# Performance work log

Hardware: AMD Instinct MI355X
Metric: run time of the kernel (lower is better)

The kernel has to match this reference:

```python
import jax, jax.numpy as jnp
import numpy as np

EPS = 1e-8
PAD = 1  # kernel // 2 for kernel=3


def setup_inputs() -> dict:
    key = jax.random.key(0)
    k1, k2, k3, k4, k5 = jax.random.split(key, 5)
    b, c, h, w = 16, 256, 64, 64
    out_ch, kernel, style_dim = 256, 3, 512
    x = jax.random.normal(k1, (b, c, h, w), dtype=jnp.float32)
    style = jax.random.normal(k2, (b, style_dim), dtype=jnp.float32)
    # learned params
    weight = jax.random.normal(k3, (1, out_ch, c, kernel, kernel), dtype=jnp.float32)
    lim = 1.0 / np.sqrt(style_dim)
    mod_w = jax.random.uniform(k4, (c, style_dim), minval=-lim, maxval=lim, dtype=jnp.float32)
    mod_b = jax.random.uniform(k5, (c,), minval=-lim, maxval=lim, dtype=jnp.float32)
    return {"x": x, "style": style, "weight": weight, "mod_w": mod_w, "mod_b": mod_b}


def reference(x, style, weight, mod_w, mod_b):
    # s[b,i]: per-sample, per-input-channel modulation from the style Linear
    s = style @ mod_w.T + mod_b                     # [b, in_ch]
    w = weight[0]                                    # [out_ch, in_ch, k, k]
    # demod factor: sum_{i,kh,kw} (w[o,i,kh,kw]*s[b,i])^2 = sum_i s^2 * sum_kk w^2
    w_sq = jnp.sum(w * w, axis=(2, 3))               # [out_ch, in_ch]
    d = jax.lax.rsqrt(jnp.einsum('oi,bi->bo', w_sq, s * s) + EPS)  # [b, out_ch]
    # modulate input channels instead of materializing per-sample weights
    xs = x * s[:, :, None, None]                     # [b, in_ch, h, w]
    y = jax.lax.conv_general_dilated(
        xs, w, window_strides=(1, 1), padding=[(PAD, PAD), (PAD, PAD)],
        dimension_numbers=('NCHW', 'OIHW', 'NCHW'))
    return y * d[:, :, None, None]                   # [b, out_ch, h, w]
```

## Files before the change

### kernel.cpp

```cpp
#include <hip/hip_runtime.h>
#include <hip/hip_bf16.h>
#include <cstdint>
#include <cstddef>

typedef __bf16 bf16_t;
typedef __bf16 bf16x4 __attribute__((ext_vector_type(4)));
typedef __bf16 bf16x8 __attribute__((ext_vector_type(8)));
typedef float  f32x4  __attribute__((ext_vector_type(4)));

#define NB   16
#define NC   256
#define NO   256
#define SD   512
#define NPIX 4096
#define CPAD 36

#define WS_S   0
#define WS_WSQ 32768
#define WS_WT  294912

__global__ __launch_bounds__(256) void prep1(
    const float* __restrict__ style, const float* __restrict__ weight,
    const float* __restrict__ mod_w, const float* __restrict__ mod_b,
    float* __restrict__ s_buf, float* __restrict__ wsq, bf16_t* __restrict__ wT)
{
    const int blk = blockIdx.x;
    const int tid = threadIdx.x;
    if (blk < 16) {
        const int b = blk, i = tid;
        const float* st = style + b * SD;
        const float* mw = mod_w + i * SD;
        float acc = 0.f;
        for (int k = 0; k < SD; k += 4) {
            float4 a = *(const float4*)(st + k);
            float4 c = *(const float4*)(mw + k);
            acc += a.x * c.x + a.y * c.y + a.z * c.z + a.w * c.w;
        }
        s_buf[b * NC + i] = acc + mod_b[i];
    } else {
        const int o = blk - 16, i = tid;
        const float* wp = weight + (o * NC + i) * 9;
        float q = 0.f;
        #pragma unroll
        for (int t = 0; t < 9; ++t) {
            float v = wp[t];
            q += v * v;
            wT[t * (NO * NC) + o * NC + i] = (bf16_t)v;
        }
        wsq[o * NC + i] = q;
    }
}

__device__ __forceinline__ void stage_a3(const bf16_t* __restrict__ wT_base,
                                         int tap0, int o0, int ic0,
                                         bf16_t* dst, int tid)
{
    #pragma unroll
    for (int t = 0; t < 3; ++t) {
        const bf16_t* wt = wT_base + (size_t)(tap0 + t) * (NO * NC);
        #pragma unroll
        for (int it = 0; it < 2; ++it) {
            int s = it * 256 + tid;
            const bf16_t* g = wt + (o0 + (s & 127)) * NC + ic0 + (s >> 7) * 8;
            __builtin_amdgcn_global_load_lds(
                (const __attribute__((address_space(1))) void*)g,
                (__attribute__((address_space(3))) void*)(dst + t * 4096 + s * 8),
                16, 0, 0);
        }
    }
}

__global__ __launch_bounds__(256, 2) void conv_mfma(
    const float* __restrict__ x,
    const bf16_t* __restrict__ wT,
    const float* __restrict__ s_buf,
    const float* __restrict__ wsq,
    float* __restrict__ out)
{
    __shared__ bf16_t lds_a[6][4096];
    __shared__ bf16_t lds_b[4 * 64 * CPAD];

    const int tid   = threadIdx.x;
    const int lane  = tid & 63;
    const int wv    = tid >> 6;
    const int wo    = wv >> 1;
    const int wp    = wv & 1;
    const int pt    = blockIdx.x;
    const int o0    = blockIdx.y * 128;
    const int batch = blockIdx.z;
    const int row0  = pt * 2;

    const int l15 = lane & 15;
    const int kg  = lane >> 4;
    const int k0  = kg * 8;

    const int colB = tid & 63;
    const int cgrp = tid >> 6;

    f32x4 acc[4][4];
    #pragma unroll
    for (int i = 0; i < 4; ++i)
        #pragma unroll
        for (int j = 0; j < 4; ++j) {
            f32x4 z = {0.f, 0.f, 0.f, 0.f};
            acc[i][j] = z;
        }

    bf16x8 bzero;
    #pragma unroll
    for (int j = 0; j < 8; ++j) bzero[j] = (bf16_t)0.f;

    bf16_t* lds_a0 = &lds_a[0][0];
    #define SUPER(idx) (lds_a0 + (size_t)((idx) & 1) * (3 * 4096))

    float vx[4][8];
    float sv[8];
    auto XLOAD = [&](int ic0) {
        const float* sp = s_buf + batch * NC + ic0 + cgrp * 8;
        float4 sa = *(const float4*)sp;
        float4 sb = *(const float4*)(sp + 4);
        sv[0]=sa.x; sv[1]=sa.y; sv[2]=sa.z; sv[3]=sa.w;
        sv[4]=sb.x; sv[5]=sb.y; sv[6]=sb.z; sv[7]=sb.w;
        const float* xbase = x + (size_t)(batch * NC + ic0 + cgrp * 8) * NPIX + colB;
        #pragma unroll
        for (int r = 0; r < 4; ++r) {
            const int gy = row0 - 1 + r;
            const bool valid = ((unsigned)gy < 64u);
            const float* rp = xbase + gy * 64;
            #pragma unroll
            for (int j = 0; j < 8; ++j)
                vx[r][j] = valid ? rp[j * NPIX] : 0.f;
        }
    };
    auto BWRITE = [&]() {
        #pragma unroll
        for (int r = 0; r < 4; ++r) {
            const int lbase = (r * 64 + colB) * CPAD + cgrp * 8;
            #pragma unroll
            for (int half = 0; half < 2; ++half) {
                union { bf16_t h[4]; uint2 u; } pk;
                #pragma unroll
                for (int j = 0; j < 4; ++j)
                    pk.h[j] = (bf16_t)(vx[r][half * 4 + j] * sv[half * 4 + j]);
                *(uint2*)&lds_b[lbase + half * 4] = pk.u;
            }
        }
    };

    stage_a3(wT, 0, o0, 0, SUPER(0), tid);
    XLOAD(0);
    BWRITE();
    __syncthreads();

    #pragma unroll 1
    for (int ch = 0; ch < 8; ++ch) {
        const int ic0 = ch * 32;

        #pragma unroll
        for (int i = 0; i < 3; ++i) {
            bf16_t* cur = SUPER(ch + i);
            bf16_t* nxt = SUPER(ch + i + 1);

            if (i < 2) {
                stage_a3(wT, 3 * (i + 1), o0, ic0, nxt, tid);
                asm volatile("s_waitcnt vmcnt(6)" ::: "memory");
            } else if (ch < 7) {
                stage_a3(wT, 0, o0, ic0 + 32, nxt, tid);
                asm volatile("s_waitcnt vmcnt(6)" ::: "memory");
            } else {
                asm volatile("s_waitcnt vmcnt(0)" ::: "memory");
            }
            __builtin_amdgcn_sched_barrier(0);

            if (i == 2 && ch < 7)
                XLOAD(ic0 + 32);

            const int r = wp + i;
            __builtin_amdgcn_s_setprio(1);
            #pragma unroll
            for (int t = 0; t < 3; ++t) {
                const bf16_t* abuf = cur + t * 4096;
                bf16x8 af[4];
                #pragma unroll
                for (int of = 0; of < 4; ++of)
                    af[of] = *(const bf16x8*)&abuf[kg * 1024 + (wo * 64 + of * 16 + l15) * 8];

                bf16x8 bfr[4];
                #pragma unroll
                for (int nf = 0; nf < 4; ++nf) {
                    const int c = nf * 16 + l15 + t - 1;
                    if ((unsigned)c < 64u) {
                        const bf16_t* p = &lds_b[(r * 64 + c) * CPAD + k0];
                        bf16x4 lo = *(const bf16x4*)p;
                        bf16x4 hi = *(const bf16x4*)(p + 4);
                        bfr[nf] = __builtin_shufflevector(lo, hi, 0, 1, 2, 3, 4, 5, 6, 7);
                    } else {
                        bfr[nf] = bzero;
                    }
                }

                #pragma unroll
                for (int of = 0; of < 4; ++of)
                    #pragma unroll
                    for (int nf = 0; nf < 4; ++nf)
                        acc[of][nf] = __builtin_amdgcn_mfma_f32_16x16x32_bf16(
                            af[of], bfr[nf], acc[of][nf], 0, 0, 0);
            }
            __builtin_amdgcn_s_setprio(0);

            if (i < 2)
                __builtin_amdgcn_s_barrier();
        }

        if (ch < 7) {
            __builtin_amdgcn_s_barrier();
            BWRITE();
            asm volatile("s_waitcnt lgkmcnt(0)" ::: "memory");
            __builtin_amdgcn_sched_barrier(0);
            __builtin_amdgcn_s_barrier();
        }
    }
    #undef SUPER

    __syncthreads();
    float* d_sh = (float*)&lds_b[0];
    {
        const int ol   = tid >> 1;
        const int half = tid & 1;
        const float* wq = wsq + (size_t)(o0 + ol) * NC + half * 128;
        const float* sb = s_buf + batch * NC + half * 128;
        float sum = 0.f;
        #pragma unroll 4
        for (int i = 0; i < 128; i += 4) {
            float4 w4 = *(const float4*)(wq + i);
            float4 s4 = *(const float4*)(sb + i);
            sum += w4.x * s4.x * s4.x + w4.y * s4.y * s4.y
                 + w4.z * s4.z * s4.z + w4.w * s4.w * s4.w;
        }
        sum += __shfl_xor(sum, 1);
        if (half == 0) d_sh[ol] = rsqrtf(sum + 1e-8f);
    }
    __syncthreads();

    const int p_base = pt * 128 + wp * 64;
    #pragma unroll
    for (int of = 0; of < 4; ++of) {
        #pragma unroll
        for (int rg = 0; rg < 4; ++rg) {
            const int o_l = wo * 64 + of * 16 + (lane >> 4) * 4 + rg;
            const float dv = d_sh[o_l];
            const size_t obase = (size_t)(batch * NO + o0 + o_l) * NPIX;
            #pragma unroll
            for (int nf = 0; nf < 4; ++nf) {
                const int p_g = p_base + nf * 16 + l15;
                out[obase + p_g] = acc[of][nf][rg] * dv;
            }
        }
    }
}

extern "C" void kernel_launch(void* const* d_in, const int* in_sizes, int n_in,
                              void* d_out, int out_size, void* d_ws, size_t ws_size,
                              hipStream_t stream)
{
    const float* x      = (const float*)d_in[0];
    const float* style  = (const float*)d_in[1];
    const float* weight = (const float*)d_in[2];
    const float* mod_w  = (const float*)d_in[3];
    const float* mod_b  = (const float*)d_in[4];
    float* out = (float*)d_out;

    char* ws = (char*)d_ws;
    float*  s_buf = (float*)(ws + WS_S);
    float*  wsq   = (float*)(ws + WS_WSQ);
    bf16_t* wT    = (bf16_t*)(ws + WS_WT);

    hipLaunchKernelGGL(prep1, dim3(272), dim3(256), 0, stream,
                       style, weight, mod_w, mod_b, s_buf, wsq, wT);
    hipLaunchKernelGGL(conv_mfma, dim3(32, 2, 16), dim3(256), 0, stream,
                       x, wT, s_buf, wsq, out);
}
```

Measured before the change: 243.1 us.

## Double block to 512 threads, splitting pixel columns across eight waves

The conv block grows from 4 to 8 wavefronts. Each wave now covers 64 output channels by 32 pixels instead of 64, which halves the accumulators and per-thread staging loads. Weight staging, x loading, the demod reduction and the epilogue are all redistributed over 512 threads, with matching vmcnt waits. This aims to raise latency hiding and lower register pressure, at the cost of more A-fragment LDS reads per MFMA and a higher launch_bounds occupancy request that may not fit LDS.

```diff
diff --git a/kernel.cpp b/kernel.cpp
--- a/kernel.cpp
+++ b/kernel.cpp
@@ -58,19 +58,16 @@
     #pragma unroll
     for (int t = 0; t < 3; ++t) {
         const bf16_t* wt = wT_base + (size_t)(tap0 + t) * (NO * NC);
-        #pragma unroll
-        for (int it = 0; it < 2; ++it) {
-            int s = it * 256 + tid;
-            const bf16_t* g = wt + (o0 + (s & 127)) * NC + ic0 + (s >> 7) * 8;
-            __builtin_amdgcn_global_load_lds(
-                (const __attribute__((address_space(1))) void*)g,
-                (__attribute__((address_space(3))) void*)(dst + t * 4096 + s * 8),
-                16, 0, 0);
-        }
-    }
-}
-
-__global__ __launch_bounds__(256, 2) void conv_mfma(
+        const int s = tid;
+        const bf16_t* g = wt + (o0 + (s & 127)) * NC + ic0 + (s >> 7) * 8;
+        __builtin_amdgcn_global_load_lds(
+            (const __attribute__((address_space(1))) void*)g,
+            (__attribute__((address_space(3))) void*)(dst + t * 4096 + s * 8),
+            16, 0, 0);
+    }
+}
+
+__global__ __launch_bounds__(512, 4) void conv_mfma(
     const float* __restrict__ x,
     const bf16_t* __restrict__ wT,
     const float* __restrict__ s_buf,
@@ -82,9 +79,10 @@
 
     const int tid   = threadIdx.x;
     const int lane  = tid & 63;
-    const int wv    = tid >> 6;
-    const int wo    = wv >> 1;
-    const int wp    = wv & 1;
+    const int wq    = tid >> 6;
+    const int wo    = wq >> 2;
+    const int prow  = (wq >> 1) & 1;
+    const int pc32  = (wq & 1) * 32;
     const int pt    = blockIdx.x;
     const int o0    = blockIdx.y * 128;
     const int batch = blockIdx.z;
@@ -97,11 +95,11 @@
     const int colB = tid & 63;
     const int cgrp = tid >> 6;
 
-    f32x4 acc[4][4];
+    f32x4 acc[4][2];
     #pragma unroll
     for (int i = 0; i < 4; ++i)
         #pragma unroll
-        for (int j = 0; j < 4; ++j) {
+        for (int j = 0; j < 2; ++j) {
             f32x4 z = {0.f, 0.f, 0.f, 0.f};
             acc[i][j] = z;
         }
@@ -113,37 +111,31 @@
     bf16_t* lds_a0 = &lds_a[0][0];
     #define SUPER(idx) (lds_a0 + (size_t)((idx) & 1) * (3 * 4096))
 
-    float vx[4][8];
-    float sv[8];
+    float vx[4][4];
+    float sv[4];
     auto XLOAD = [&](int ic0) {
-        const float* sp = s_buf + batch * NC + ic0 + cgrp * 8;
+        const float* sp = s_buf + batch * NC + ic0 + cgrp * 4;
         float4 sa = *(const float4*)sp;
-        float4 sb = *(const float4*)(sp + 4);
-        sv[0]=sa.x; sv[1]=sa.y; sv[2]=sa.z; sv[3]=sa.w;
-        sv[4]=sb.x; sv[5]=sb.y; sv[6]=sb.z; sv[7]=sb.w;
-        const float* xbase = x + (size_t)(batch * NC + ic0 + cgrp * 8) * NPIX + colB;
+        sv[0] = sa.x; sv[1] = sa.y; sv[2] = sa.z; sv[3] = sa.w;
+        const float* xbase = x + (size_t)(batch * NC + ic0 + cgrp * 4) * NPIX + colB;
         #pragma unroll
         for (int r = 0; r < 4; ++r) {
             const int gy = row0 - 1 + r;
             const bool valid = ((unsigned)gy < 64u);
             const float* rp = xbase + gy * 64;
             #pragma unroll
-            for (int j = 0; j < 8; ++j)
+            for (int j = 0; j < 4; ++j)
                 vx[r][j] = valid ? rp[j * NPIX] : 0.f;
         }
     };
     auto BWRITE = [&]() {
         #pragma unroll
         for (int r = 0; r < 4; ++r) {
-            const int lbase = (r * 64 + colB) * CPAD + cgrp * 8;
-            #pragma unroll
-            for (int half = 0; half < 2; ++half) {
-                union { bf16_t h[4]; uint2 u; } pk;
-                #pragma unroll
-                for (int j = 0; j < 4; ++j)
-                    pk.h[j] = (bf16_t)(vx[r][half * 4 + j] * sv[half * 4 + j]);
-                *(uint2*)&lds_b[lbase + half * 4] = pk.u;
-            }
+            union { bf16_t h[4]; uint2 u; } pk;
+            #pragma unroll
+            for (int j = 0; j < 4; ++j)
+                pk.h[j] = (bf16_t)(vx[r][j] * sv[j]);
+            *(uint2*)&lds_b[(r * 64 + colB) * CPAD + cgrp * 4] = pk.u;
         }
     };
 
@@ -163,10 +155,10 @@
 
             if (i < 2) {
                 stage_a3(wT, 3 * (i + 1), o0, ic0, nxt, tid);
-                asm volatile("s_waitcnt vmcnt(6)" ::: "memory");
+                asm volatile("s_waitcnt vmcnt(3)" ::: "memory");
             } else if (ch < 7) {
                 stage_a3(wT, 0, o0, ic0 + 32, nxt, tid);
-                asm volatile("s_waitcnt vmcnt(6)" ::: "memory");
+                asm volatile("s_waitcnt vmcnt(3)" ::: "memory");
             } else {
                 asm volatile("s_waitcnt vmcnt(0)" ::: "memory");
             }
@@ -175,7 +167,7 @@
             if (i == 2 && ch < 7)
                 XLOAD(ic0 + 32);
 
-            const int r = wp + i;
+            const int r = prow + i;
             __builtin_amdgcn_s_setprio(1);
             #pragma unroll
             for (int t = 0; t < 3; ++t) {
@@ -185,10 +177,10 @@
                 for (int of = 0; of < 4; ++of)
                     af[of] = *(const bf16x8*)&abuf[kg * 1024 + (wo * 64 + of * 16 + l15) * 8];
 
-                bf16x8 bfr[4];
+                bf16x8 bfr[2];
                 #pragma unroll
-                for (int nf = 0; nf < 4; ++nf) {
-                    const int c = nf * 16 + l15 + t - 1;
+                for (int nf = 0; nf < 2; ++nf) {
+                    const int c = pc32 + nf * 16 + l15 + t - 1;
                     if ((unsigned)c < 64u) {
                         const bf16_t* p = &lds_b[(r * 64 + c) * CPAD + k0];
                         bf16x4 lo = *(const bf16x4*)p;
@@ -202,7 +194,7 @@
                 #pragma unroll
                 for (int of = 0; of < 4; ++of)
                     #pragma unroll
-                    for (int nf = 0; nf < 4; ++nf)
+                    for (int nf = 0; nf < 2; ++nf)
                         acc[of][nf] = __builtin_amdgcn_mfma_f32_16x16x32_bf16(
                             af[of], bfr[nf], acc[of][nf], 0, 0, 0);
             }
@@ -225,34 +217,35 @@
     __syncthreads();
     float* d_sh = (float*)&lds_b[0];
     {
-        const int ol   = tid >> 1;
-        const int half = tid & 1;
-        const float* wq = wsq + (size_t)(o0 + ol) * NC + half * 128;
-        const float* sb = s_buf + batch * NC + half * 128;
+        const int ol = tid >> 2;
+        const int q  = tid & 3;
+        const float* wq_p = wsq + (size_t)(o0 + ol) * NC + q * 64;
+        const float* sb   = s_buf + batch * NC + q * 64;
         float sum = 0.f;
         #pragma unroll 4
-        for (int i = 0; i < 128; i += 4) {
-            float4 w4 = *(const float4*)(wq + i);
+        for (int i = 0; i < 64; i += 4) {
+            float4 w4 = *(const float4*)(wq_p + i);
             float4 s4 = *(const float4*)(sb + i);
             sum += w4.x * s4.x * s4.x + w4.y * s4.y * s4.y
                  + w4.z * s4.z * s4.z + w4.w * s4.w * s4.w;
         }
         sum += __shfl_xor(sum, 1);
-        if (half == 0) d_sh[ol] = rsqrtf(sum + 1e-8f);
+        sum += __shfl_xor(sum, 2);
+        if (q == 0) d_sh[ol] = rsqrtf(sum + 1e-8f);
     }
     __syncthreads();
 
-    const int p_base = pt * 128 + wp * 64;
+    const int prow_g = row0 + prow;
     #pragma unroll
     for (int of = 0; of < 4; ++of) {
         #pragma unroll
         for (int rg = 0; rg < 4; ++rg) {
-            const int o_l = wo * 64 + of * 16 + (lane >> 4) * 4 + rg;
+            const int o_l = wo * 64 + of * 16 + kg * 4 + rg;
             const float dv = d_sh[o_l];
             const size_t obase = (size_t)(batch * NO + o0 + o_l) * NPIX;
             #pragma unroll
-            for (int nf = 0; nf < 4; ++nf) {
-                const int p_g = p_base + nf * 16 + l15;
+            for (int nf = 0; nf < 2; ++nf) {
+                const int p_g = prow_g * 64 + pc32 + nf * 16 + l15;
                 out[obase + p_g] = acc[of][nf][rg] * dv;
             }
         }
@@ -277,6 +270,6 @@
 
     hipLaunchKernelGGL(prep1, dim3(272), dim3(256), 0, stream,
                        style, weight, mod_w, mod_b, s_buf, wsq, wT);
-    hipLaunchKernelGGL(conv_mfma, dim3(32, 2, 16), dim3(256), 0, stream,
+    hipLaunchKernelGGL(conv_mfma, dim3(32, 2, 16), dim3(512), 0, stream,
                        x, wT, s_buf, wsq, out);
 }
```

After: 254.5 us. +4.7%, slower.

## Enlarge conv tile to all output channels and four rows per 512-thread block

Applied to the files above, without the earlier changes.

Each conv block now covers all 256 output channels and 4 image rows, using 8 waves instead of 4. Every wave holds an 8x4 grid of MFMA accumulators instead of 4x4. The aim is to reuse each staged weight tile across more pixels and each modulated input tile across all output channels, cutting global and LDS staging traffic per FLOP. The grid shrinks to 256 blocks, about one per CU, and LDS use rises to roughly 126 KB. That risks lower occupancy, more register pressure and less latency hiding.

```diff
diff --git a/kernel.cpp b/kernel.cpp
--- a/kernel.cpp
+++ b/kernel.cpp
@@ -52,43 +52,41 @@
 }
 
 __device__ __forceinline__ void stage_a3(const bf16_t* __restrict__ wT_base,
-                                         int tap0, int o0, int ic0,
-                                         bf16_t* dst, int tid)
+                                         int tap0, int ic0, bf16_t* dst, int tid)
 {
     #pragma unroll
     for (int t = 0; t < 3; ++t) {
         const bf16_t* wt = wT_base + (size_t)(tap0 + t) * (NO * NC);
         #pragma unroll
         for (int it = 0; it < 2; ++it) {
-            int s = it * 256 + tid;
-            const bf16_t* g = wt + (o0 + (s & 127)) * NC + ic0 + (s >> 7) * 8;
+            int s = it * 512 + tid;
+            const bf16_t* g = wt + (s & 255) * NC + ic0 + (s >> 8) * 8;
             __builtin_amdgcn_global_load_lds(
                 (const __attribute__((address_space(1))) void*)g,
-                (__attribute__((address_space(3))) void*)(dst + t * 4096 + s * 8),
+                (__attribute__((address_space(3))) void*)(dst + t * 8192 + s * 8),
                 16, 0, 0);
         }
     }
 }
 
-__global__ __launch_bounds__(256, 2) void conv_mfma(
+__global__ __launch_bounds__(512, 2) void conv_mfma(
     const float* __restrict__ x,
     const bf16_t* __restrict__ wT,
     const float* __restrict__ s_buf,
     const float* __restrict__ wsq,
     float* __restrict__ out)
 {
-    __shared__ bf16_t lds_a[6][4096];
-    __shared__ bf16_t lds_b[4 * 64 * CPAD];
+    __shared__ bf16_t lds_a[2][3 * 8192];
+    __shared__ bf16_t lds_b[6 * 64 * CPAD];
 
     const int tid   = threadIdx.x;
     const int lane  = tid & 63;
-    const int wv    = tid >> 6;
-    const int wo    = wv >> 1;
-    const int wp    = wv & 1;
+    const int wqv   = tid >> 6;
+    const int wo    = wqv & 1;
+    const int wp    = wqv >> 1;
     const int pt    = blockIdx.x;
-    const int o0    = blockIdx.y * 128;
     const int batch = blockIdx.z;
-    const int row0  = pt * 2;
+    const int row0  = pt * 4;
 
     const int l15 = lane & 15;
     const int kg  = lane >> 4;
@@ -97,9 +95,9 @@
     const int colB = tid & 63;
     const int cgrp = tid >> 6;
 
-    f32x4 acc[4][4];
-    #pragma unroll
-    for (int i = 0; i < 4; ++i)
+    f32x4 acc[8][4];
+    #pragma unroll
+    for (int i = 0; i < 8; ++i)
         #pragma unroll
         for (int j = 0; j < 4; ++j) {
             f32x4 z = {0.f, 0.f, 0.f, 0.f};
@@ -111,43 +109,37 @@
     for (int j = 0; j < 8; ++j) bzero[j] = (bf16_t)0.f;
 
     bf16_t* lds_a0 = &lds_a[0][0];
-    #define SUPER(idx) (lds_a0 + (size_t)((idx) & 1) * (3 * 4096))
-
-    float vx[4][8];
-    float sv[8];
+    #define SUPER(idx) (lds_a0 + (size_t)((idx) & 1) * (3 * 8192))
+
+    float vx[6][4];
+    float sv[4];
     auto XLOAD = [&](int ic0) {
-        const float* sp = s_buf + batch * NC + ic0 + cgrp * 8;
+        const float* sp = s_buf + batch * NC + ic0 + cgrp * 4;
         float4 sa = *(const float4*)sp;
-        float4 sb = *(const float4*)(sp + 4);
-        sv[0]=sa.x; sv[1]=sa.y; sv[2]=sa.z; sv[3]=sa.w;
-        sv[4]=sb.x; sv[5]=sb.y; sv[6]=sb.z; sv[7]=sb.w;
-        const float* xbase = x + (size_t)(batch * NC + ic0 + cgrp * 8) * NPIX + colB;
-        #pragma unroll
-        for (int r = 0; r < 4; ++r) {
+        sv[0] = sa.x; sv[1] = sa.y; sv[2] = sa.z; sv[3] = sa.w;
+        const float* xbase = x + (size_t)(batch * NC + ic0 + cgrp * 4) * NPIX + colB;
+        #pragma unroll
+        for (int r = 0; r < 6; ++r) {
             const int gy = row0 - 1 + r;
             const bool valid = ((unsigned)gy < 64u);
             const float* rp = xbase + gy * 64;
             #pragma unroll
-            for (int j = 0; j < 8; ++j)
+            for (int j = 0; j < 4; ++j)
                 vx[r][j] = valid ? rp[j * NPIX] : 0.f;
         }
     };
     auto BWRITE = [&]() {
         #pragma unroll
-        for (int r = 0; r < 4; ++r) {
-            const int lbase = (r * 64 + colB) * CPAD + cgrp * 8;
-            #pragma unroll
-            for (int half = 0; half < 2; ++half) {
-                union { bf16_t h[4]; uint2 u; } pk;
-                #pragma unroll
-                for (int j = 0; j < 4; ++j)
-                    pk.h[j] = (bf16_t)(vx[r][half * 4 + j] * sv[half * 4 + j]);
-                *(uint2*)&lds_b[lbase + half * 4] = pk.u;
-            }
+        for (int r = 0; r < 6; ++r) {
+            union { bf16_t h[4]; uint2 u; } pk;
+            #pragma unroll
+            for (int j = 0; j < 4; ++j)
+                pk.h[j] = (bf16_t)(vx[r][j] * sv[j]);
+            *(uint2*)&lds_b[(r * 64 + colB) * CPAD + cgrp * 4] = pk.u;
         }
     };
 
-    stage_a3(wT, 0, o0, 0, SUPER(0), tid);
+    stage_a3(wT, 0, 0, SUPER(0), tid);
     XLOAD(0);
     BWRITE();
     __syncthreads();
@@ -158,14 +150,14 @@
 
         #pragma unroll
         for (int i = 0; i < 3; ++i) {
-            bf16_t* cur = SUPER(ch + i);
+            const bf16_t* cur = SUPER(ch + i);
             bf16_t* nxt = SUPER(ch + i + 1);
 
             if (i < 2) {
-                stage_a3(wT, 3 * (i + 1), o0, ic0, nxt, tid);
+                stage_a3(wT, 3 * (i + 1), ic0, nxt, tid);
                 asm volatile("s_waitcnt vmcnt(6)" ::: "memory");
             } else if (ch < 7) {
-                stage_a3(wT, 0, o0, ic0 + 32, nxt, tid);
+                stage_a3(wT, 0, ic0 + 32, nxt, tid);
                 asm volatile("s_waitcnt vmcnt(6)" ::: "memory");
             } else {
                 asm volatile("s_waitcnt vmcnt(0)" ::: "memory");
@@ -179,11 +171,11 @@
             __builtin_amdgcn_s_setprio(1);
             #pragma unroll
             for (int t = 0; t < 3; ++t) {
-                const bf16_t* abuf = cur + t * 4096;
-                bf16x8 af[4];
+                const bf16_t* abuf = cur + t * 8192;
+                bf16x8 af[8];
                 #pragma unroll
-                for (int of = 0; of < 4; ++of)
-                    af[of] = *(const bf16x8*)&abuf[kg * 1024 + (wo * 64 + of * 16 + l15) * 8];
+                for (int of = 0; of < 8; ++of)
+                    af[of] = *(const bf16x8*)&abuf[kg * 2048 + (wo * 128 + of * 16 + l15) * 8];
 
                 bf16x8 bfr[4];
                 #pragma unroll
@@ -200,7 +192,7 @@
                 }
 
                 #pragma unroll
-                for (int of = 0; of < 4; ++of)
+                for (int of = 0; of < 8; ++of)
                     #pragma unroll
                     for (int nf = 0; nf < 4; ++nf)
                         acc[of][nf] = __builtin_amdgcn_mfma_f32_16x16x32_bf16(
@@ -227,12 +219,12 @@
     {
         const int ol   = tid >> 1;
         const int half = tid & 1;
-        const float* wq = wsq + (size_t)(o0 + ol) * NC + half * 128;
-        const float* sb = s_buf + batch * NC + half * 128;
+        const float* wq_p = wsq + (size_t)ol * NC + half * 128;
+        const float* sb   = s_buf + batch * NC + half * 128;
         float sum = 0.f;
         #pragma unroll 4
         for (int i = 0; i < 128; i += 4) {
-            float4 w4 = *(const float4*)(wq + i);
+            float4 w4 = *(const float4*)(wq_p + i);
             float4 s4 = *(const float4*)(sb + i);
             sum += w4.x * s4.x * s4.x + w4.y * s4.y * s4.y
                  + w4.z * s4.z * s4.z + w4.w * s4.w * s4.w;
@@ -242,17 +234,17 @@
     }
     __syncthreads();
 
-    const int p_base = pt * 128 + wp * 64;
-    #pragma unroll
-    for (int of = 0; of < 4; ++of) {
+    const int prow_g = row0 + wp;
+    #pragma unroll
+    for (int of = 0; of < 8; ++of) {
         #pragma unroll
         for (int rg = 0; rg < 4; ++rg) {
-            const int o_l = wo * 64 + of * 16 + (lane >> 4) * 4 + rg;
+            const int o_l = wo * 128 + of * 16 + kg * 4 + rg;
             const float dv = d_sh[o_l];
-            const size_t obase = (size_t)(batch * NO + o0 + o_l) * NPIX;
+            const size_t obase = (size_t)(batch * NO + o_l) * NPIX;
             #pragma unroll
             for (int nf = 0; nf < 4; ++nf) {
-                const int p_g = p_base + nf * 16 + l15;
+                const int p_g = prow_g * 64 + nf * 16 + l15;
                 out[obase + p_g] = acc[of][nf][rg] * dv;
             }
         }
@@ -277,6 +269,6 @@
 
     hipLaunchKernelGGL(prep1, dim3(272), dim3(256), 0, stream,
                        style, weight, mod_w, mod_b, s_buf, wsq, wT);
-    hipLaunchKernelGGL(conv_mfma, dim3(32, 2, 16), dim3(256), 0, stream,
+    hipLaunchKernelGGL(conv_mfma, dim3(16, 1, 16), dim3(512), 0, stream,
                        x, wT, s_buf, wsq, out);
 }
```

Result: slower. 383.6 us (+57.8%).
